# Performance work log

Hardware: AMD Instinct MI355X
Metric: run time of the kernel (lower is better)

Reference implementation:

```python
import jax, jax.numpy as jnp
import numpy as np

TOKENS, IN_F, OUT_F = 8192, 4096, 4096


def setup_inputs() -> dict:
    key = jax.random.key(0)
    k1, k2 = jax.random.split(key)
    return {
        "input": jax.random.normal(k1, (TOKENS, IN_F), dtype=jnp.float32),
        "weight": jax.random.normal(k2, (OUT_F, IN_F), dtype=jnp.float32),
        "weight_scale": jnp.ones((1,), dtype=jnp.float32),
        "input_scale": jnp.ones((1,), dtype=jnp.float32),
    }


def reference(input, weight, weight_scale, input_scale):
    # BitNet-style: ternary weight quantization {-1, 0, +1} w.r.t. learned scale,
    # int8-range activation quantization, fused dequant-scaled matmul.
    ws = weight_scale[0]
    xs = input_scale[0]
    # quantize_weights: round(w / ws) clipped to ternary
    w_q = jnp.clip(jnp.round(weight / ws), -1.0, 1.0)          # [out, in], values in {-1,0,1}
    # fused_quantize_matmul: quantize activations to int8 range, matmul, dequant scale
    x_q = jnp.clip(jnp.round(input / xs), -128.0, 127.0)        # [tokens, in]
    out = jnp.einsum('ti,oi->to', x_q, w_q) * (xs * ws)         # [tokens, out]
    return out
```

## Files before the change

### kernel.cpp

```cpp
#include <hip/hip_runtime.h>
#include <hip/hip_bf16.h>
#include <stdint.h>


typedef int int4v __attribute__((ext_vector_type(4)));

typedef __attribute__((address_space(1))) void gvoid;
typedef __attribute__((address_space(3))) void lvoid;

#define M_DIM 8192
#define N_DIM 4096
#define K_DIM 4096

#define BM 128
#define BN 128
#define BK 64

__global__ __launch_bounds__(256) void quant_kernel(
    const float* __restrict__ in, int8_t* __restrict__ out,
    const float* __restrict__ scale_ptr, float lo, float hi, long n) {
  long i = ((long)blockIdx.x * blockDim.x + threadIdx.x) * 16;
  if (i >= n) return;
  float s = scale_ptr[0];
  float4 a = *(const float4*)(in + i);
  float4 b = *(const float4*)(in + i + 4);
  float4 c = *(const float4*)(in + i + 8);
  float4 d = *(const float4*)(in + i + 12);
  float v[16] = {a.x, a.y, a.z, a.w, b.x, b.y, b.z, b.w,
                 c.x, c.y, c.z, c.w, d.x, d.y, d.z, d.w};
  union { int8_t c[16]; int4 q; } u;
#pragma unroll
  for (int t = 0; t < 16; ++t) {
    float q = rintf(v[t] / s);
    q = fminf(fmaxf(q, lo), hi);
    u.c[t] = (int8_t)q;
  }
  *(int4*)(out + i) = u.q;
}

__global__ __launch_bounds__(256) void gemm_bt(
    const int8_t* __restrict__ A,
    const int8_t* __restrict__ B,
    float* __restrict__ C,
    const float* __restrict__ ws_ptr, const float* __restrict__ xs_ptr) {
  __shared__ __attribute__((aligned(16))) char smem[2 * BM * BK];
  char* sA = smem;
  char* sB = smem + BM * BK;

  const int tid  = threadIdx.x;
  const int wave = tid >> 6;
  const int lane = tid & 63;
  const int wr   = wave >> 1;
  const int wc   = wave & 1;
  const int fr   = lane & 15;
  const int quad = lane >> 4;

  const long m0 = (long)blockIdx.y * BM;
  const long n0 = (long)blockIdx.x * BN;

  const int srow = wave * 32 + (lane >> 2);
  const int scol = (lane & 3) * 16;
  const int8_t* gA = A + (m0 + srow) * K_DIM + scol;
  const int8_t* gB = B + (n0 + srow) * K_DIM + scol;
  char* lA0 = sA + wave * 2048;
  char* lA1 = sA + wave * 2048 + 1024;
  char* lB0 = sB + wave * 2048;
  char* lB1 = sB + wave * 2048 + 1024;

  int4v acc[4][4] = {};

  for (int k0 = 0; k0 < K_DIM; k0 += BK) {
    __builtin_amdgcn_global_load_lds((gvoid*)(gA),               (lvoid*)lA0, 16, 0, 0);
    __builtin_amdgcn_global_load_lds((gvoid*)(gA + 16 * K_DIM),  (lvoid*)lA1, 16, 0, 0);
    __builtin_amdgcn_global_load_lds((gvoid*)(gB),               (lvoid*)lB0, 16, 0, 0);
    __builtin_amdgcn_global_load_lds((gvoid*)(gB + 16 * K_DIM),  (lvoid*)lB1, 16, 0, 0);
    gA += BK;
    gB += BK;
    __syncthreads();

    int4v a_frag[4], b_frag[4];
#pragma unroll
    for (int i = 0; i < 4; ++i) {
      a_frag[i] = *(const int4v*)(sA + (wr * 64 + i * 16 + fr) * BK + quad * 16);
      b_frag[i] = *(const int4v*)(sB + (wc * 64 + i * 16 + fr) * BK + quad * 16);
    }
#pragma unroll
    for (int i = 0; i < 4; ++i)
#pragma unroll
      for (int j = 0; j < 4; ++j)
        acc[i][j] = __builtin_amdgcn_mfma_i32_16x16x64_i8(a_frag[i], b_frag[j], acc[i][j], 0, 0, 0);

    __syncthreads();
  }

  const float s = ws_ptr[0] * xs_ptr[0];
#pragma unroll
  for (int i = 0; i < 4; ++i) {
    const long row0 = m0 + wr * 64 + i * 16 + quad * 4;
#pragma unroll
    for (int j = 0; j < 4; ++j) {
      const long col = n0 + wc * 64 + j * 16 + fr;
#pragma unroll
      for (int r = 0; r < 4; ++r) {
        C[(row0 + r) * N_DIM + col] = (float)acc[i][j][r] * s;
      }
    }
  }
}

extern "C" void kernel_launch(void* const* d_in, const int* in_sizes, int n_in,
                              void* d_out, int out_size, void* d_ws, size_t ws_size,
                              hipStream_t stream) {
  const float* x  = (const float*)d_in[0];
  const float* w  = (const float*)d_in[1];
  const float* ws = (const float*)d_in[2];
  const float* xs = (const float*)d_in[3];
  float* out = (float*)d_out;

  int8_t* xq = (int8_t*)d_ws;
  int8_t* wq = (int8_t*)d_ws + (size_t)M_DIM * K_DIM;

  const long n_x = (long)M_DIM * K_DIM;
  const long n_w = (long)N_DIM * K_DIM;

  quant_kernel<<<(n_x / 16 + 255) / 256, 256, 0, stream>>>(x, xq, xs, -128.f, 127.f, n_x);
  quant_kernel<<<(n_w / 16 + 255) / 256, 256, 0, stream>>>(w, wq, ws, -1.f, 1.f, n_w);

  dim3 grid(N_DIM / BN, M_DIM / BM);
  gemm_bt<<<grid, 256, 0, stream>>>(xq, wq, out, ws, xs);
}
```

Baseline: 411.9 us.

## Switch GEMM to 32x32x32 int8 MFMA with BK=128 and XOR-swizzled LDS

```diff
diff --git a/kernel.cpp b/kernel.cpp
--- a/kernel.cpp
+++ b/kernel.cpp
@@ -3,7 +3,8 @@
 #include <stdint.h>
 
 
-typedef int int4v __attribute__((ext_vector_type(4)));
+typedef int  int4v  __attribute__((ext_vector_type(4)));
+typedef int  int16v __attribute__((ext_vector_type(16)));
 
 typedef __attribute__((address_space(1))) void gvoid;
 typedef __attribute__((address_space(3))) void lvoid;
@@ -14,7 +15,7 @@
 
 #define BM 128
 #define BN 128
-#define BK 64
+#define BK 128
 
 __global__ __launch_bounds__(256) void quant_kernel(
     const float* __restrict__ in, int8_t* __restrict__ out,
@@ -52,57 +53,63 @@
   const int lane = tid & 63;
   const int wr   = wave >> 1;
   const int wc   = wave & 1;
-  const int fr   = lane & 15;
-  const int quad = lane >> 4;
+  const int r    = lane & 31;
+  const int half = lane >> 5;
 
   const long m0 = (long)blockIdx.y * BM;
   const long n0 = (long)blockIdx.x * BN;
 
-  const int srow = wave * 32 + (lane >> 2);
-  const int scol = (lane & 3) * 16;
-  const int8_t* gA = A + (m0 + srow) * K_DIM + scol;
-  const int8_t* gB = B + (n0 + srow) * K_DIM + scol;
-  char* lA0 = sA + wave * 2048;
-  char* lA1 = sA + wave * 2048 + 1024;
-  char* lB0 = sB + wave * 2048;
-  char* lB1 = sB + wave * 2048 + 1024;
+  const int srow   = wave * 32 + (lane >> 3);
+  const int schunk = ((lane & 7) ^ (lane >> 3)) * 16;
+  const int8_t* gA = A + (m0 + srow) * K_DIM + schunk;
+  const int8_t* gB = B + (n0 + srow) * K_DIM + schunk;
+  char* lA = sA + wave * 4096;
+  char* lB = sB + wave * 4096;
 
-  int4v acc[4][4] = {};
+  int16v acc[2][2] = {};
 
   for (int k0 = 0; k0 < K_DIM; k0 += BK) {
-    __builtin_amdgcn_global_load_lds((gvoid*)(gA),               (lvoid*)lA0, 16, 0, 0);
-    __builtin_amdgcn_global_load_lds((gvoid*)(gA + 16 * K_DIM),  (lvoid*)lA1, 16, 0, 0);
-    __builtin_amdgcn_global_load_lds((gvoid*)(gB),               (lvoid*)lB0, 16, 0, 0);
-    __builtin_amdgcn_global_load_lds((gvoid*)(gB + 16 * K_DIM),  (lvoid*)lB1, 16, 0, 0);
+#pragma unroll
+    for (int t = 0; t < 4; ++t)
+      __builtin_amdgcn_global_load_lds((gvoid*)(gA + t * 8 * K_DIM),
+                                       (lvoid*)(lA + t * 1024), 16, 0, 0);
+#pragma unroll
+    for (int t = 0; t < 4; ++t)
+      __builtin_amdgcn_global_load_lds((gvoid*)(gB + t * 8 * K_DIM),
+                                       (lvoid*)(lB + t * 1024), 16, 0, 0);
     gA += BK;
     gB += BK;
     __syncthreads();
 
-    int4v a_frag[4], b_frag[4];
+    const int arow = (wr * 64 + r) * BK;
+    const int brow = (wc * 64 + r) * BK;
 #pragma unroll
-    for (int i = 0; i < 4; ++i) {
-      a_frag[i] = *(const int4v*)(sA + (wr * 64 + i * 16 + fr) * BK + quad * 16);
-      b_frag[i] = *(const int4v*)(sB + (wc * 64 + i * 16 + fr) * BK + quad * 16);
+    for (int ks = 0; ks < 4; ++ks) {
+      const int co = (((ks * 2 + half) ^ (lane & 7)) * 16);
+      int4v a0 = *(const int4v*)(sA + arow + co);
+      int4v a1 = *(const int4v*)(sA + arow + 32 * BK + co);
+      int4v b0 = *(const int4v*)(sB + brow + co);
+      int4v b1 = *(const int4v*)(sB + brow + 32 * BK + co);
+      acc[0][0] = __builtin_amdgcn_mfma_i32_32x32x32_i8(a0, b0, acc[0][0], 0, 0, 0);
+      acc[0][1] = __builtin_amdgcn_mfma_i32_32x32x32_i8(a0, b1, acc[0][1], 0, 0, 0);
+      acc[1][0] = __builtin_amdgcn_mfma_i32_32x32x32_i8(a1, b0, acc[1][0], 0, 0, 0);
+      acc[1][1] = __builtin_amdgcn_mfma_i32_32x32x32_i8(a1, b1, acc[1][1], 0, 0, 0);
     }
-#pragma unroll
-    for (int i = 0; i < 4; ++i)
-#pragma unroll
-      for (int j = 0; j < 4; ++j)
-        acc[i][j] = __builtin_amdgcn_mfma_i32_16x16x64_i8(a_frag[i], b_frag[j], acc[i][j], 0, 0, 0);
 
     __syncthreads();
   }
 
   const float s = ws_ptr[0] * xs_ptr[0];
 #pragma unroll
-  for (int i = 0; i < 4; ++i) {
-    const long row0 = m0 + wr * 64 + i * 16 + quad * 4;
+  for (int mb = 0; mb < 2; ++mb) {
 #pragma unroll
-    for (int j = 0; j < 4; ++j) {
-      const long col = n0 + wc * 64 + j * 16 + fr;
+    for (int nb = 0; nb < 2; ++nb) {
+      const long col = n0 + wc * 64 + nb * 32 + r;
+      const long rowbase = m0 + wr * 64 + mb * 32 + 4 * half;
 #pragma unroll
-      for (int r = 0; r < 4; ++r) {
-        C[(row0 + r) * N_DIM + col] = (float)acc[i][j][r] * s;
+      for (int reg = 0; reg < 16; ++reg) {
+        const long row = rowbase + (reg & 3) + 8 * (reg >> 2);
+        C[row * N_DIM + col] = (float)acc[mb][nb][reg] * s;
       }
     }
   }
```

New measurement: 389.8 us. -5.4%, faster.
